# Optimization experiments

Hardware: AMD Instinct MI355X
Metric: run time of the kernel (lower is better)

Reference implementation:

```python
import jax, jax.numpy as jnp
import numpy as np

B, T, D, H = 4, 2048, 1024, 16
HD = D // H  # head dim = 64


def setup_inputs() -> dict:
    key = jax.random.key(0)
    ks = jax.random.split(key, 12)
    s = 1.0 / np.sqrt(D)
    inp = {
        "Q": jax.random.normal(ks[0], (B, T, D), jnp.float32),
        "K": jax.random.normal(ks[1], (B, T, D), jnp.float32),
        "V": jax.random.normal(ks[2], (B, T, D), jnp.float32),
        "mask": jnp.tril(jnp.ones((T, T), jnp.int32))[None, None],  # causal [1,1,T,T]
        "Wq": jax.random.normal(ks[3], (D, D), jnp.float32) * s,
        "bq": jax.random.normal(ks[4], (D,), jnp.float32) * s,
        "Wk": jax.random.normal(ks[5], (D, D), jnp.float32) * s,
        "bk": jax.random.normal(ks[6], (D,), jnp.float32) * s,
        "Wv": jax.random.normal(ks[7], (D, D), jnp.float32) * s,
        "bv": jax.random.normal(ks[8], (D,), jnp.float32) * s,
        "Wo": jax.random.normal(ks[9], (D, D), jnp.float32) * s,
        "bo": jax.random.normal(ks[10], (D,), jnp.float32) * s,
    }
    return inp


def reference(Q, K, V, mask, Wq, bq, Wk, bk, Wv, bv, Wo, bo):
    b, t, d = Q.shape
    # projections (torch Linear: x @ W^T + b)
    q = (Q @ Wq.T + bq).reshape(b, t, H, HD).transpose(0, 2, 1, 3)  # [b,h,t,hd]
    k = (K @ Wk.T + bk).reshape(b, t, H, HD).transpose(0, 2, 1, 3)
    v = (V @ Wv.T + bv).reshape(b, t, H, HD).transpose(0, 2, 1, 3)
    score = jnp.einsum("bhqd,bhkd->bhqk", q, k) / jnp.sqrt(jnp.float32(HD))
    score = jnp.where(mask == 0, jnp.float32(-1e9), score)
    attn = jax.nn.softmax(score, axis=-1)
    out = jnp.einsum("bhqk,bhkd->bhqd", attn, v)
    out = out.transpose(0, 2, 1, 3).reshape(b, t, d)
    return out @ Wo.T + bo
```

## Files before the change

### kernel.cpp

```cpp
#include <hip/hip_runtime.h>
#include <stdint.h>

#define B_SZ  4
#define T_SEQ 2048
#define DIM   1024
#define NH    16
#define HD    64
#define M_TOT (B_SZ * T_SEQ)

typedef unsigned short u16;
typedef unsigned long long u64;
typedef __attribute__((ext_vector_type(8))) __bf16 bf16x8;
typedef __attribute__((ext_vector_type(4))) float  floatx4;
typedef __attribute__((ext_vector_type(16))) float floatx16;

#define SCL_Q (0.125f * 1.44269504089f)

__device__ __forceinline__ u16 f2bf(float f) {
  union { float f; uint32_t u; } v; v.f = f;
  uint32_t r = v.u + 0x7fffu + ((v.u >> 16) & 1u);
  return (u16)(r >> 16);
}

__device__ __forceinline__ void gl_lds16(const void* g, void* l) {
  __builtin_amdgcn_global_load_lds(
      (const __attribute__((address_space(1))) uint32_t*)g,
      (__attribute__((address_space(3))) uint32_t*)l, 16, 0, 0);
}

__global__ __launch_bounds__(256) void cvt_all(
    const float* __restrict__ s0, const float* __restrict__ s1,
    const float* __restrict__ s2, const float* __restrict__ s3,
    const float* __restrict__ s4, const float* __restrict__ s5,
    const float* __restrict__ s6,
    u16* __restrict__ d0, u16* __restrict__ d1, u16* __restrict__ d2,
    u16* __restrict__ d3, u16* __restrict__ d4, u16* __restrict__ d5,
    u16* __restrict__ d6) {
  const float* s; u16* d; int n;
  switch (blockIdx.y) {
    case 0: s = s0; d = d0; n = DIM * DIM; break;
    case 1: s = s1; d = d1; n = DIM * DIM; break;
    case 2: s = s2; d = d2; n = DIM * DIM; break;
    case 3: s = s3; d = d3; n = DIM * DIM; break;
    case 4: s = s4; d = d4; n = M_TOT * DIM; break;
    case 5: s = s5; d = d5; n = M_TOT * DIM; break;
    default: s = s6; d = d6; n = M_TOT * DIM; break;
  }
  int i = (blockIdx.x * 256 + threadIdx.x) * 8;
  if (i >= n) return;
  float4 a = *(const float4*)(s + i);
  float4 b = *(const float4*)(s + i + 4);
  uint4 o;
  o.x = (uint32_t)f2bf(a.x) | ((uint32_t)f2bf(a.y) << 16);
  o.y = (uint32_t)f2bf(a.z) | ((uint32_t)f2bf(a.w) << 16);
  o.z = (uint32_t)f2bf(b.x) | ((uint32_t)f2bf(b.y) << 16);
  o.w = (uint32_t)f2bf(b.z) | ((uint32_t)f2bf(b.w) << 16);
  *(uint4*)(d + i) = o;
}

#define BKG 64
__global__ __launch_bounds__(256) void gemm_qkv(
    const u16* __restrict__ Qb, const u16* __restrict__ Kb,
    const u16* __restrict__ Vb,
    const u16* __restrict__ Wq, const u16* __restrict__ Wk,
    const u16* __restrict__ Wv,
    const float* __restrict__ bq, const float* __restrict__ bk,
    const float* __restrict__ bv,
    u16* __restrict__ qo, u16* __restrict__ ko, u16* __restrict__ vo) {
  const u16* A; const u16* Bw; const float* bias; u16* Co;
  if (blockIdx.z == 0)      { A = Qb; Bw = Wq; bias = bq; Co = qo; }
  else if (blockIdx.z == 1) { A = Kb; Bw = Wk; bias = bk; Co = ko; }
  else                      { A = Vb; Bw = Wv; bias = bv; Co = vo; }

  __shared__ u16 As[128 * 64];
  __shared__ u16 Bs[128 * 64];

  const int tid  = threadIdx.x;
  const int wave = tid >> 6, lane = tid & 63;
  const int quad = lane >> 4, l16 = lane & 15;
  const int wm = wave >> 1, wn = wave & 1;
  const int m0 = blockIdx.x * 128, n0 = blockIdx.y * 128;

  const floatx4 FZ = {0.f, 0.f, 0.f, 0.f};
  floatx4 acc[4][4];
#pragma unroll
  for (int mt = 0; mt < 4; ++mt)
#pragma unroll
    for (int nt = 0; nt < 4; ++nt) acc[mt][nt] = FZ;

  for (int k0 = 0; k0 < DIM; k0 += BKG) {
    __syncthreads();
#pragma unroll
    for (int j = 0; j < 4; ++j) {
      int pc = j * 256 + tid;
      int r = pc >> 3, c = pc & 7;
      int sc = c ^ (r & 7);
      gl_lds16(A  + (size_t)(m0 + r) * DIM + k0 + sc * 8,
               &As[(j * 256 + wave * 64) * 8]);
      gl_lds16(Bw + (size_t)(n0 + r) * DIM + k0 + sc * 8,
               &Bs[(j * 256 + wave * 64) * 8]);
    }
    __syncthreads();

#pragma unroll
    for (int kk = 0; kk < 2; ++kk) {
      bf16x8 af[4], bfr[4];
#pragma unroll
      for (int mt = 0; mt < 4; ++mt) {
        int ra = wm * 64 + mt * 16 + l16;
        af[mt] = *(const bf16x8*)&As[ra * 64 + (((kk * 4 + quad) ^ (ra & 7)) * 8)];
      }
#pragma unroll
      for (int nt = 0; nt < 4; ++nt) {
        int rb = wn * 64 + nt * 16 + l16;
        bfr[nt] = *(const bf16x8*)&Bs[rb * 64 + (((kk * 4 + quad) ^ (rb & 7)) * 8)];
      }
#pragma unroll
      for (int mt = 0; mt < 4; ++mt)
#pragma unroll
        for (int nt = 0; nt < 4; ++nt)
          acc[mt][nt] = __builtin_amdgcn_mfma_f32_16x16x32_bf16(
              af[mt], bfr[nt], acc[mt][nt], 0, 0, 0);
    }
  }

  if (blockIdx.z == 2) {
#pragma unroll
    for (int nt = 0; nt < 4; ++nt) {
      int n = n0 + wn * 64 + nt * 16 + l16;
      float bb = bias[n];
      int h = n >> 6, hd = n & 63;
#pragma unroll
      for (int mt = 0; mt < 4; ++mt) {
        int mbase = m0 + wm * 64 + mt * 16 + quad * 4;
        int b = mbase >> 11, t = mbase & (T_SEQ - 1);
        u64 pk = 0;
#pragma unroll
        for (int r = 0; r < 4; ++r)
          pk |= (u64)f2bf(acc[mt][nt][r] + bb) << (16 * r);
        *(u64*)&Co[((size_t)((b * NH + h) * HD + hd)) * T_SEQ + t] = pk;
      }
    }
  } else {
    const float sc = (blockIdx.z == 0) ? SCL_Q : 1.0f;
#pragma unroll
    for (int nt = 0; nt < 4; ++nt) {
      int n = n0 + wn * 64 + nt * 16 + l16;
      float bb = bias[n];
      int h = n >> 6, hd = n & 63;
#pragma unroll
      for (int mt = 0; mt < 4; ++mt) {
#pragma unroll
        for (int r = 0; r < 4; ++r) {
          int m = m0 + wm * 64 + mt * 16 + quad * 4 + r;
          int b = m >> 11, t = m & (T_SEQ - 1);
          Co[((size_t)(b * NH + h) * T_SEQ + t) * HD + hd] =
              f2bf((acc[mt][nt][r] + bb) * sc);
        }
      }
    }
  }
}

__global__ __launch_bounds__(512, 2) void flash_attn(
    const u16* __restrict__ qp, const u16* __restrict__ kp,
    const u16* __restrict__ vp, u16* __restrict__ ao) {
  const int bh = blockIdx.x;
  const int y = blockIdx.y;
  const int qt = (y < 4) ? (7 - y) : (y - 4);
  const int b = bh >> 4, h = bh & 15;
  const u16* Qg = qp + (size_t)bh * T_SEQ * HD;
  const u16* Kg = kp + (size_t)bh * T_SEQ * HD;
  const u16* Vg = vp + (size_t)bh * HD * T_SEQ;

  __shared__ u16 lds[6][64 * 64];

  const int tid = threadIdx.x, wave = tid >> 6, lane = tid & 63;
  const int hi = lane >> 5, c31 = lane & 31;
  const int lr8 = lane >> 3, lc8 = lane & 7;

  const int qrow = qt * 256 + wave * 32 + c31;

  bf16x8 bq[4];
#pragma unroll
  for (int cth = 0; cth < 4; ++cth)
    bq[cth] = *(const bf16x8*)(Qg + (size_t)qrow * HD + cth * 16 + hi * 8);

  const int nkb = 4 * qt + 4;
  const int srow = wave * 8 + lr8;
  const int ssc = lc8 ^ (srow & 7);

  gl_lds16(Kg + (size_t)srow * HD + ssc * 8, &lds[0][wave * 8 * 64]);
  gl_lds16(Vg + (size_t)srow * T_SEQ + ssc * 8, &lds[1][wave * 8 * 64]);
  gl_lds16(Kg + (size_t)(64 + srow) * HD + ssc * 8, &lds[2][wave * 8 * 64]);
  gl_lds16(Vg + (size_t)srow * T_SEQ + 64 + ssc * 8, &lds[3][wave * 8 * 64]);

  asm volatile("" :: "v"(bq[0]), "v"(bq[1]), "v"(bq[2]), "v"(bq[3]));

  floatx16 o0, o1;
#pragma unroll
  for (int i = 0; i < 16; ++i) { o0[i] = 0.f; o1[i] = 0.f; }
  float l_p = 0.f;

  int koff[4];
#pragma unroll
  for (int x = 0; x < 4; ++x)
    koff[x] = c31 * 64 + (((x * 2 + hi) ^ (c31 & 7)) * 8);

  const int qwmin = qt * 256 + wave * 32;
  const int qwmax = qwmin + 31;
  int pc_ = 0;
  int ps_ = 2;
  for (int kb = 0; kb < nkb; ++kb) {
    if (kb + 1 < nkb) asm volatile("s_waitcnt vmcnt(2)" ::: "memory");
    else              asm volatile("s_waitcnt vmcnt(0)" ::: "memory");
    __builtin_amdgcn_s_barrier();
    __builtin_amdgcn_sched_barrier(0);

    if (kb + 2 < nkb) {
      const u16* Kgk = Kg + (size_t)(kb + 2) * 64 * HD;
      const u16* Vgk = Vg + (size_t)(kb + 2) * 64;
      gl_lds16(Kgk + (size_t)srow * HD + ssc * 8, &lds[ps_ * 2][wave * 8 * 64]);
      gl_lds16(Vgk + (size_t)srow * T_SEQ + ssc * 8,
               &lds[ps_ * 2 + 1][wave * 8 * 64]);
      ps_ = (ps_ == 2) ? 0 : ps_ + 1;
    }

    if (kb * 64 <= qwmax) {
      const u16* Ks = &lds[pc_ * 2][0];
      const u16* Vs = &lds[pc_ * 2 + 1][0];

      floatx16 s0, s1;
#pragma unroll
      for (int i = 0; i < 16; ++i) { s0[i] = 0.f; s1[i] = 0.f; }
#pragma unroll
      for (int cth = 0; cth < 4; ++cth) {
        bf16x8 ka = *(const bf16x8*)&Ks[koff[cth]];
        bf16x8 kb2 = *(const bf16x8*)&Ks[koff[cth] + 32 * 64];
        s0 = __builtin_amdgcn_mfma_f32_32x32x16_bf16(ka, bq[cth], s0, 0, 0, 0);
        s1 = __builtin_amdgcn_mfma_f32_32x32x16_bf16(kb2, bq[cth], s1, 0, 0, 0);
      }

      if (kb * 64 + 63 > qwmin) {
        int kvb = kb * 64 + 4 * hi;
#pragma unroll
        for (int r = 0; r < 16; ++r) {
          int kvr = kvb + (r & 3) + 8 * (r >> 2);
          if (kvr > qrow)      s0[r] = -3e38f;
          if (kvr + 32 > qrow) s1[r] = -3e38f;
        }
      }

      uint32_t pk0[8], pk1[8];
      float rs = 0.f;
#pragma unroll
      for (int rr = 0; rr < 8; ++rr) {
        union { float f; uint32_t u; } x0, x1, y0, y1;
        x0.f = __builtin_amdgcn_exp2f(s0[2 * rr]);
        x1.f = __builtin_amdgcn_exp2f(s0[2 * rr + 1]);
        y0.f = __builtin_amdgcn_exp2f(s1[2 * rr]);
        y1.f = __builtin_amdgcn_exp2f(s1[2 * rr + 1]);
        rs += (x0.f + x1.f) + (y0.f + y1.f);
        pk0[rr] = __builtin_amdgcn_perm(x1.u, x0.u, 0x07060302);
        pk1[rr] = __builtin_amdgcn_perm(y1.u, y0.u, 0x07060302);
      }
      l_p += rs;

#pragma unroll
      for (int cc = 0; cc < 4; ++cc) {
        const uint32_t* pks = (cc & 2) ? pk1 : pk0;
        const int e4 = (cc & 1) * 4;
        auto r0 = __builtin_amdgcn_permlane32_swap(pks[e4 + 0], pks[e4 + 2],
                                                   false, false);
        auto r1 = __builtin_amdgcn_permlane32_swap(pks[e4 + 1], pks[e4 + 3],
                                                   false, false);
        union { uint32_t u[4]; bf16x8 v; } bp;
        bp.u[0] = r0[0]; bp.u[1] = r1[0]; bp.u[2] = r0[1]; bp.u[3] = r1[1];
        bf16x8 va = *(const bf16x8*)&Vs[koff[cc]];
        bf16x8 vb = *(const bf16x8*)&Vs[koff[cc] + 32 * 64];
        o0 = __builtin_amdgcn_mfma_f32_32x32x16_bf16(va, bp.v, o0, 0, 0, 0);
        o1 = __builtin_amdgcn_mfma_f32_32x32x16_bf16(vb, bp.v, o1, 0, 0, 0);
      }
    }
    pc_ = (pc_ == 2) ? 0 : pc_ + 1;
  }

  {
    float l = l_p + __shfl_xor(l_p, 32);
    float inv = 1.0f / l;
    const size_t obase = (size_t)(b * T_SEQ + qrow) * DIM + h * HD;
#pragma unroll
    for (int u4 = 0; u4 < 4; ++u4) {
      u64 w0 = 0, w1 = 0;
#pragma unroll
      for (int r = 0; r < 4; ++r) {
        w0 |= (u64)f2bf(o0[4 * u4 + r] * inv) << (16 * r);
        w1 |= (u64)f2bf(o1[4 * u4 + r] * inv) << (16 * r);
      }
      *(u64*)&ao[obase + 8 * u4 + 4 * hi] = w0;
      *(u64*)&ao[obase + 32 + 8 * u4 + 4 * hi] = w1;
    }
  }
}

__global__ __launch_bounds__(256) void gemm_out(
    const u16* __restrict__ Ain, const u16* __restrict__ Wo,
    const float* __restrict__ bo, float* __restrict__ out) {
  __shared__ u16 As[128 * 64];
  __shared__ u16 Bs[128 * 64];

  const int tid  = threadIdx.x;
  const int wave = tid >> 6, lane = tid & 63;
  const int quad = lane >> 4, l16 = lane & 15;
  const int wm = wave >> 1, wn = wave & 1;
  const int m0 = blockIdx.x * 128, n0 = blockIdx.y * 128;

  const floatx4 FZ = {0.f, 0.f, 0.f, 0.f};
  floatx4 acc[4][4];
#pragma unroll
  for (int mt = 0; mt < 4; ++mt)
#pragma unroll
    for (int nt = 0; nt < 4; ++nt) acc[mt][nt] = FZ;

  for (int k0 = 0; k0 < DIM; k0 += BKG) {
    __syncthreads();
#pragma unroll
    for (int j = 0; j < 4; ++j) {
      int pc = j * 256 + tid;
      int r = pc >> 3, c = pc & 7;
      int sc = c ^ (r & 7);
      gl_lds16(Ain + (size_t)(m0 + r) * DIM + k0 + sc * 8,
               &As[(j * 256 + wave * 64) * 8]);
      gl_lds16(Wo  + (size_t)(n0 + r) * DIM + k0 + sc * 8,
               &Bs[(j * 256 + wave * 64) * 8]);
    }
    __syncthreads();

#pragma unroll
    for (int kk = 0; kk < 2; ++kk) {
      bf16x8 af[4], bfr[4];
#pragma unroll
      for (int mt = 0; mt < 4; ++mt) {
        int ra = wm * 64 + mt * 16 + l16;
        af[mt] = *(const bf16x8*)&As[ra * 64 + (((kk * 4 + quad) ^ (ra & 7)) * 8)];
      }
#pragma unroll
      for (int nt = 0; nt < 4; ++nt) {
        int rb = wn * 64 + nt * 16 + l16;
        bfr[nt] = *(const bf16x8*)&Bs[rb * 64 + (((kk * 4 + quad) ^ (rb & 7)) * 8)];
      }
#pragma unroll
      for (int mt = 0; mt < 4; ++mt)
#pragma unroll
        for (int nt = 0; nt < 4; ++nt)
          acc[mt][nt] = __builtin_amdgcn_mfma_f32_16x16x32_bf16(
              af[mt], bfr[nt], acc[mt][nt], 0, 0, 0);
    }
  }

#pragma unroll
  for (int nt = 0; nt < 4; ++nt) {
    int n = n0 + wn * 64 + nt * 16 + l16;
    float bb = bo[n];
#pragma unroll
    for (int mt = 0; mt < 4; ++mt)
#pragma unroll
      for (int r = 0; r < 4; ++r) {
        int m = m0 + wm * 64 + mt * 16 + quad * 4 + r;
        out[(size_t)m * DIM + n] = acc[mt][nt][r] + bb;
      }
  }
}

extern "C" void kernel_launch(void* const* d_in, const int* in_sizes, int n_in,
                              void* d_out, int out_size, void* d_ws,
                              size_t ws_size, hipStream_t stream) {
  const float* Q  = (const float*)d_in[0];
  const float* K  = (const float*)d_in[1];
  const float* V  = (const float*)d_in[2];
  const float* Wq = (const float*)d_in[4];
  const float* bq = (const float*)d_in[5];
  const float* Wk = (const float*)d_in[6];
  const float* bk = (const float*)d_in[7];
  const float* Wv = (const float*)d_in[8];
  const float* bv = (const float*)d_in[9];
  const float* Wo = (const float*)d_in[10];
  const float* bo = (const float*)d_in[11];
  float* out = (float*)d_out;

  u16* wqb = (u16*)d_ws;
  u16* wkb = wqb + 1048576;
  u16* wvb = wkb + 1048576;
  u16* wob = wvb + 1048576;
  u16* Qb  = wob + 1048576;
  u16* Kb  = Qb + (size_t)M_TOT * DIM;
  u16* Vb  = Kb + (size_t)M_TOT * DIM;
  u16* qp  = Vb + (size_t)M_TOT * DIM;
  u16* kp  = qp + (size_t)M_TOT * DIM;
  u16* vp  = kp + (size_t)M_TOT * DIM;
  u16* aop = vp + (size_t)M_TOT * DIM;

  cvt_all<<<dim3(M_TOT * DIM / 2048, 7), 256, 0, stream>>>(
      Wq, Wk, Wv, Wo, Q, K, V, wqb, wkb, wvb, wob, Qb, Kb, Vb);

  gemm_qkv<<<dim3(M_TOT / 128, DIM / 128, 3), 256, 0, stream>>>(
      Qb, Kb, Vb, wqb, wkb, wvb, bq, bk, bv, qp, kp, vp);

  flash_attn<<<dim3(B_SZ * NH, T_SEQ / 256), 512, 0, stream>>>(qp, kp, vp, aop);

  gemm_out<<<dim3(M_TOT / 128, DIM / 128), 256, 0, stream>>>(aop, wob, bo, out);
}
```

Measured before the change: 309.2 us.

## Rewrite QKV projection GEMM with 256x256 tiles and double-buffered async prefetch

The QKV projection GEMM moves from 128x128 tiles with 256 threads and a load-sync-compute loop to 256x256 tiles with 512 threads. It now double-buffers LDS for A and B and issues global-to-LDS loads for the next K-steps while the current step's MFMAs run. Each K-step is split into four phases with explicit barriers, waitcnts and setprio, meant to hide memory latency and raise operand reuse per loaded byte. In exchange it uses 128KB of LDS per block and launches only 384 blocks, which risks poor CU fill and a partial last wave.

Measured after the change: 324.3 us. 4.9% more time.

```diff
diff --git a/kernel.cpp b/kernel.cpp
--- a/kernel.cpp
+++ b/kernel.cpp
@@ -58,8 +58,22 @@
   *(uint4*)(d + i) = o;
 }
 
-#define BKG 64
-__global__ __launch_bounds__(256) void gemm_qkv(
+#define BKG  64
+#define NT_K (DIM / BKG)
+
+__device__ __forceinline__ void stage_half(
+    const u16* __restrict__ src, int grow0, int k0, u16* ldsbase,
+    int wave, int lr8, int lc8) {
+#pragma unroll
+  for (int j = 0; j < 2; ++j) {
+    int rb = j * 64 + wave * 8;
+    int R  = grow0 + rb + lr8;
+    gl_lds16(src + (size_t)R * DIM + k0 + ((lc8 ^ lr8) * 8),
+             ldsbase + (size_t)rb * 64);
+  }
+}
+
+__global__ __launch_bounds__(512, 2) void gemm_qkv(
     const u16* __restrict__ Qb, const u16* __restrict__ Kb,
     const u16* __restrict__ Vb,
     const u16* __restrict__ Wq, const u16* __restrict__ Wk,
@@ -72,55 +86,97 @@
   else if (blockIdx.z == 1) { A = Kb; Bw = Wk; bias = bk; Co = ko; }
   else                      { A = Vb; Bw = Wv; bias = bv; Co = vo; }
 
-  __shared__ u16 As[128 * 64];
-  __shared__ u16 Bs[128 * 64];
+  __shared__ u16 sh[4 * 256 * 64];
+  u16* const Ab0 = sh;
+  u16* const Ab1 = sh + 256 * 64;
+  u16* const Bb0 = sh + 2 * 256 * 64;
+  u16* const Bb1 = sh + 3 * 256 * 64;
 
   const int tid  = threadIdx.x;
   const int wave = tid >> 6, lane = tid & 63;
   const int quad = lane >> 4, l16 = lane & 15;
-  const int wm = wave >> 1, wn = wave & 1;
-  const int m0 = blockIdx.x * 128, n0 = blockIdx.y * 128;
+  const int lr8 = lane >> 3, lc8 = lane & 7;
+  const int wm = wave >> 2, wn = wave & 3;
+  const int m0 = blockIdx.x * 256, n0 = blockIdx.y * 256;
 
   const floatx4 FZ = {0.f, 0.f, 0.f, 0.f};
-  floatx4 acc[4][4];
-#pragma unroll
-  for (int mt = 0; mt < 4; ++mt)
+  floatx4 acc[8][4];
+#pragma unroll
+  for (int mt = 0; mt < 8; ++mt)
 #pragma unroll
     for (int nt = 0; nt < 4; ++nt) acc[mt][nt] = FZ;
 
-  for (int k0 = 0; k0 < DIM; k0 += BKG) {
-    __syncthreads();
-#pragma unroll
-    for (int j = 0; j < 4; ++j) {
-      int pc = j * 256 + tid;
-      int r = pc >> 3, c = pc & 7;
-      int sc = c ^ (r & 7);
-      gl_lds16(A  + (size_t)(m0 + r) * DIM + k0 + sc * 8,
-               &As[(j * 256 + wave * 64) * 8]);
-      gl_lds16(Bw + (size_t)(n0 + r) * DIM + k0 + sc * 8,
-               &Bs[(j * 256 + wave * 64) * 8]);
-    }
-    __syncthreads();
-
-#pragma unroll
-    for (int kk = 0; kk < 2; ++kk) {
-      bf16x8 af[4], bfr[4];
-#pragma unroll
-      for (int mt = 0; mt < 4; ++mt) {
-        int ra = wm * 64 + mt * 16 + l16;
-        af[mt] = *(const bf16x8*)&As[ra * 64 + (((kk * 4 + quad) ^ (ra & 7)) * 8)];
-      }
-#pragma unroll
-      for (int nt = 0; nt < 4; ++nt) {
-        int rb = wn * 64 + nt * 16 + l16;
-        bfr[nt] = *(const bf16x8*)&Bs[rb * 64 + (((kk * 4 + quad) ^ (rb & 7)) * 8)];
-      }
+  stage_half(A,  m0,       0,   Ab0,            wave, lr8, lc8);
+  stage_half(A,  m0 + 128, 0,   Ab0 + 128 * 64, wave, lr8, lc8);
+  stage_half(Bw, n0,       0,   Bb0,            wave, lr8, lc8);
+  stage_half(Bw, n0 + 128, 0,   Bb0 + 128 * 64, wave, lr8, lc8);
+  stage_half(A,  m0,       BKG, Ab1,            wave, lr8, lc8);
+  stage_half(A,  m0 + 128, BKG, Ab1 + 128 * 64, wave, lr8, lc8);
+  asm volatile("s_waitcnt vmcnt(4)" ::: "memory");
+  __builtin_amdgcn_s_barrier();
+  __builtin_amdgcn_sched_barrier(0);
+
+  bf16x8 afr[4][2];
+  bf16x8 bfr[2][2];
+
+  for (int t = 0; t < NT_K; ++t) {
+    u16* const Ac = (t & 1) ? Ab1 : Ab0;
+    u16* const Bc = (t & 1) ? Bb1 : Bb0;
+    u16* const An = (t & 1) ? Ab1 : Ab0;
+    u16* const Bn = (t & 1) ? Bb0 : Bb1;
+
+#pragma unroll
+    for (int ph = 0; ph < 4; ++ph) {
+      const int mq = ph >> 1, nq = ph & 1;
+      if (nq == 0) {
+#pragma unroll
+        for (int mt = 0; mt < 4; ++mt) {
+          int ra = wm * 128 + mq * 64 + mt * 16 + l16;
+#pragma unroll
+          for (int kk = 0; kk < 2; ++kk)
+            afr[mt][kk] = *(const bf16x8*)
+                &Ac[ra * 64 + (((kk * 4 + quad) ^ (ra & 7)) * 8)];
+        }
+      }
+#pragma unroll
+      for (int nt = 0; nt < 2; ++nt) {
+        int rb = wn * 64 + nq * 32 + nt * 16 + l16;
+#pragma unroll
+        for (int kk = 0; kk < 2; ++kk)
+          bfr[nt][kk] = *(const bf16x8*)
+              &Bc[rb * 64 + (((kk * 4 + quad) ^ (rb & 7)) * 8)];
+      }
+      if (ph == 0 && t + 1 < NT_K)
+        stage_half(Bw, n0,       (t + 1) * BKG, Bn,            wave, lr8, lc8);
+      if (ph == 1 && t + 1 < NT_K)
+        stage_half(Bw, n0 + 128, (t + 1) * BKG, Bn + 128 * 64, wave, lr8, lc8);
+      if (ph == 3 && t + 2 < NT_K) {
+        stage_half(A, m0,       (t + 2) * BKG, An,            wave, lr8, lc8);
+        stage_half(A, m0 + 128, (t + 2) * BKG, An + 128 * 64, wave, lr8, lc8);
+      }
+      __builtin_amdgcn_s_barrier();
+      __builtin_amdgcn_sched_barrier(0);
+      asm volatile("s_waitcnt lgkmcnt(0)" ::: "memory");
+      __builtin_amdgcn_sched_barrier(0);
+      __builtin_amdgcn_s_setprio(1);
 #pragma unroll
       for (int mt = 0; mt < 4; ++mt)
 #pragma unroll
-        for (int nt = 0; nt < 4; ++nt)
-          acc[mt][nt] = __builtin_amdgcn_mfma_f32_16x16x32_bf16(
-              af[mt], bfr[nt], acc[mt][nt], 0, 0, 0);
+        for (int nt = 0; nt < 2; ++nt)
+#pragma unroll
+          for (int kk = 0; kk < 2; ++kk)
+            acc[mq * 4 + mt][nq * 2 + nt] =
+                __builtin_amdgcn_mfma_f32_16x16x32_bf16(
+                    afr[mt][kk], bfr[nt][kk], acc[mq * 4 + mt][nq * 2 + nt],
+                    0, 0, 0);
+      __builtin_amdgcn_s_setprio(0);
+      if (ph == 3) {
+        if (t + 1 >= NT_K) break;
+        if (t + 2 < NT_K) asm volatile("s_waitcnt vmcnt(4)" ::: "memory");
+        else              asm volatile("s_waitcnt vmcnt(0)" ::: "memory");
+      }
+      __builtin_amdgcn_s_barrier();
+      __builtin_amdgcn_sched_barrier(0);
     }
   }
 
@@ -129,16 +185,16 @@
     for (int nt = 0; nt < 4; ++nt) {
       int n = n0 + wn * 64 + nt * 16 + l16;
       float bb = bias[n];
-      int h = n >> 6, hd = n & 63;
-#pragma unroll
-      for (int mt = 0; mt < 4; ++mt) {
-        int mbase = m0 + wm * 64 + mt * 16 + quad * 4;
-        int b = mbase >> 11, t = mbase & (T_SEQ - 1);
+      int hh = n >> 6, hd = n & 63;
+#pragma unroll
+      for (int mt = 0; mt < 8; ++mt) {
+        int mbase = m0 + wm * 128 + mt * 16 + quad * 4;
+        int b = mbase >> 11, tq = mbase & (T_SEQ - 1);
         u64 pk = 0;
 #pragma unroll
         for (int r = 0; r < 4; ++r)
           pk |= (u64)f2bf(acc[mt][nt][r] + bb) << (16 * r);
-        *(u64*)&Co[((size_t)((b * NH + h) * HD + hd)) * T_SEQ + t] = pk;
+        *(u64*)&Co[((size_t)((b * NH + hh) * HD + hd)) * T_SEQ + tq] = pk;
       }
     }
   } else {
@@ -147,14 +203,14 @@
     for (int nt = 0; nt < 4; ++nt) {
       int n = n0 + wn * 64 + nt * 16 + l16;
       float bb = bias[n];
-      int h = n >> 6, hd = n & 63;
-#pragma unroll
-      for (int mt = 0; mt < 4; ++mt) {
+      int hh = n >> 6, hd = n & 63;
+#pragma unroll
+      for (int mt = 0; mt < 8; ++mt) {
 #pragma unroll
         for (int r = 0; r < 4; ++r) {
-          int m = m0 + wm * 64 + mt * 16 + quad * 4 + r;
-          int b = m >> 11, t = m & (T_SEQ - 1);
-          Co[((size_t)(b * NH + h) * T_SEQ + t) * HD + hd] =
+          int m = m0 + wm * 128 + mt * 16 + quad * 4 + r;
+          int b = m >> 11, tq = m & (T_SEQ - 1);
+          Co[((size_t)(b * NH + hh) * T_SEQ + tq) * HD + hd] =
               f2bf((acc[mt][nt][r] + bb) * sc);
         }
       }
@@ -403,7 +459,7 @@
   cvt_all<<<dim3(M_TOT * DIM / 2048, 7), 256, 0, stream>>>(
       Wq, Wk, Wv, Wo, Q, K, V, wqb, wkb, wvb, wob, Qb, Kb, Vb);
 
-  gemm_qkv<<<dim3(M_TOT / 128, DIM / 128, 3), 256, 0, stream>>>(
+  gemm_qkv<<<dim3(M_TOT / 256, DIM / 256, 3), 512, 0, stream>>>(
       Qb, Kb, Vb, wqb, wkb, wvb, bq, bk, bv, qp, kp, vp);
 
   flash_attn<<<dim3(B_SZ * NH, T_SEQ / 256), 512, 0, stream>>>(qp, kp, vp, aop);
```

## Process two 32-row query tiles per wave in flash attention, halving waves

Applied to the files above, without the earlier changes.

Each wave of the flash attention kernel now handles 64 query rows (two 32-row MFMA tiles) instead of 32, and the block shrinks from 512 to 256 threads. Every K and V fragment read from LDS then feeds four MFMAs instead of two, which halves LDS read traffic per unit of compute and halves barrier participants. Each thread now issues two K/V staging loads per buffer. The cost is roughly double the accumulator and score registers per wave, which may cut occupancy or cause spills, and fewer waves per block to hide latency.

After: 308.2 us (median of 3 runs). About the same (-0.3%).

```diff
diff --git a/kernel.cpp b/kernel.cpp
--- a/kernel.cpp
+++ b/kernel.cpp
@@ -162,7 +162,7 @@
   }
 }
 
-__global__ __launch_bounds__(512, 2) void flash_attn(
+__global__ __launch_bounds__(256, 2) void flash_attn(
     const u16* __restrict__ qp, const u16* __restrict__ kp,
     const u16* __restrict__ vp, u16* __restrict__ ao) {
   const int bh = blockIdx.x;
@@ -179,126 +179,164 @@
   const int hi = lane >> 5, c31 = lane & 31;
   const int lr8 = lane >> 3, lc8 = lane & 7;
 
-  const int qrow = qt * 256 + wave * 32 + c31;
-
-  bf16x8 bq[4];
-#pragma unroll
-  for (int cth = 0; cth < 4; ++cth)
-    bq[cth] = *(const bf16x8*)(Qg + (size_t)qrow * HD + cth * 16 + hi * 8);
+  const int wbase = qt * 256 + wave * 64;
+  const int qrowA = wbase + c31;
+  const int qrowB = qrowA + 32;
+
+  bf16x8 bqA[4], bqB[4];
+#pragma unroll
+  for (int cth = 0; cth < 4; ++cth) {
+    bqA[cth] = *(const bf16x8*)(Qg + (size_t)qrowA * HD + cth * 16 + hi * 8);
+    bqB[cth] = *(const bf16x8*)(Qg + (size_t)qrowB * HD + cth * 16 + hi * 8);
+  }
 
   const int nkb = 4 * qt + 4;
-  const int srow = wave * 8 + lr8;
-  const int ssc = lc8 ^ (srow & 7);
-
-  gl_lds16(Kg + (size_t)srow * HD + ssc * 8, &lds[0][wave * 8 * 64]);
-  gl_lds16(Vg + (size_t)srow * T_SEQ + ssc * 8, &lds[1][wave * 8 * 64]);
-  gl_lds16(Kg + (size_t)(64 + srow) * HD + ssc * 8, &lds[2][wave * 8 * 64]);
-  gl_lds16(Vg + (size_t)srow * T_SEQ + 64 + ssc * 8, &lds[3][wave * 8 * 64]);
-
-  asm volatile("" :: "v"(bq[0]), "v"(bq[1]), "v"(bq[2]), "v"(bq[3]));
-
-  floatx16 o0, o1;
-#pragma unroll
-  for (int i = 0; i < 16; ++i) { o0[i] = 0.f; o1[i] = 0.f; }
-  float l_p = 0.f;
+
+#define STAGE_KV(kbidx, bufpair)                                              \
+  {                                                                           \
+    const u16* Kgk = Kg + (size_t)(kbidx) * 64 * HD;                          \
+    const u16* Vgk = Vg + (size_t)(kbidx) * 64;                               \
+    _Pragma("unroll") for (int i_ = 0; i_ < 2; ++i_) {                        \
+      int r_ = i_ * 32 + wave * 8 + lr8;                                      \
+      int sc_ = lc8 ^ (r_ & 7);                                               \
+      gl_lds16(Kgk + (size_t)r_ * HD + sc_ * 8,                               \
+               &lds[(bufpair) * 2][(i_ * 32 + wave * 8) * 64]);               \
+      gl_lds16(Vgk + (size_t)r_ * T_SEQ + sc_ * 8,                            \
+               &lds[(bufpair) * 2 + 1][(i_ * 32 + wave * 8) * 64]);           \
+    }                                                                         \
+  }
+
+  STAGE_KV(0, 0);
+  STAGE_KV(1, 1);
+
+  asm volatile("" :: "v"(bqA[0]), "v"(bqA[1]), "v"(bqA[2]), "v"(bqA[3]),
+                     "v"(bqB[0]), "v"(bqB[1]), "v"(bqB[2]), "v"(bqB[3]));
+
+  floatx16 oA0, oA1, oB0, oB1;
+#pragma unroll
+  for (int i = 0; i < 16; ++i) { oA0[i] = 0.f; oA1[i] = 0.f;
+                                 oB0[i] = 0.f; oB1[i] = 0.f; }
+  float l_pA = 0.f, l_pB = 0.f;
 
   int koff[4];
 #pragma unroll
   for (int x = 0; x < 4; ++x)
     koff[x] = c31 * 64 + (((x * 2 + hi) ^ (c31 & 7)) * 8);
 
-  const int qwmin = qt * 256 + wave * 32;
-  const int qwmax = qwmin + 31;
-  int pc_ = 0;
-  int ps_ = 2;
+  int pcb = 0;
+  int psb = 2;
   for (int kb = 0; kb < nkb; ++kb) {
-    if (kb + 1 < nkb) asm volatile("s_waitcnt vmcnt(2)" ::: "memory");
+    if (kb + 1 < nkb) asm volatile("s_waitcnt vmcnt(4)" ::: "memory");
     else              asm volatile("s_waitcnt vmcnt(0)" ::: "memory");
     __builtin_amdgcn_s_barrier();
     __builtin_amdgcn_sched_barrier(0);
 
     if (kb + 2 < nkb) {
-      const u16* Kgk = Kg + (size_t)(kb + 2) * 64 * HD;
-      const u16* Vgk = Vg + (size_t)(kb + 2) * 64;
-      gl_lds16(Kgk + (size_t)srow * HD + ssc * 8, &lds[ps_ * 2][wave * 8 * 64]);
-      gl_lds16(Vgk + (size_t)srow * T_SEQ + ssc * 8,
-               &lds[ps_ * 2 + 1][wave * 8 * 64]);
-      ps_ = (ps_ == 2) ? 0 : ps_ + 1;
-    }
-
-    if (kb * 64 <= qwmax) {
-      const u16* Ks = &lds[pc_ * 2][0];
-      const u16* Vs = &lds[pc_ * 2 + 1][0];
-
-      floatx16 s0, s1;
-#pragma unroll
-      for (int i = 0; i < 16; ++i) { s0[i] = 0.f; s1[i] = 0.f; }
+      STAGE_KV(kb + 2, psb);
+      psb = (psb == 2) ? 0 : psb + 1;
+    }
+
+    if (kb * 64 <= wbase + 63) {
+      const u16* Ks = &lds[pcb * 2][0];
+      const u16* Vs = &lds[pcb * 2 + 1][0];
+
+      floatx16 sA0, sA1, sB0, sB1;
+#pragma unroll
+      for (int i = 0; i < 16; ++i) { sA0[i] = 0.f; sA1[i] = 0.f;
+                                     sB0[i] = 0.f; sB1[i] = 0.f; }
 #pragma unroll
       for (int cth = 0; cth < 4; ++cth) {
         bf16x8 ka = *(const bf16x8*)&Ks[koff[cth]];
-        bf16x8 kb2 = *(const bf16x8*)&Ks[koff[cth] + 32 * 64];
-        s0 = __builtin_amdgcn_mfma_f32_32x32x16_bf16(ka, bq[cth], s0, 0, 0, 0);
-        s1 = __builtin_amdgcn_mfma_f32_32x32x16_bf16(kb2, bq[cth], s1, 0, 0, 0);
-      }
-
-      if (kb * 64 + 63 > qwmin) {
+        bf16x8 kh = *(const bf16x8*)&Ks[koff[cth] + 32 * 64];
+        sA0 = __builtin_amdgcn_mfma_f32_32x32x16_bf16(ka, bqA[cth], sA0, 0, 0, 0);
+        sA1 = __builtin_amdgcn_mfma_f32_32x32x16_bf16(kh, bqA[cth], sA1, 0, 0, 0);
+        sB0 = __builtin_amdgcn_mfma_f32_32x32x16_bf16(ka, bqB[cth], sB0, 0, 0, 0);
+        sB1 = __builtin_amdgcn_mfma_f32_32x32x16_bf16(kh, bqB[cth], sB1, 0, 0, 0);
+      }
+
+      if (kb * 64 + 63 > wbase) {
         int kvb = kb * 64 + 4 * hi;
 #pragma unroll
         for (int r = 0; r < 16; ++r) {
           int kvr = kvb + (r & 3) + 8 * (r >> 2);
-          if (kvr > qrow)      s0[r] = -3e38f;
-          if (kvr + 32 > qrow) s1[r] = -3e38f;
+          if (kvr > qrowA)      sA0[r] = -3e38f;
+          if (kvr + 32 > qrowA) sA1[r] = -3e38f;
+          if (kvr > qrowB)      sB0[r] = -3e38f;
+          if (kvr + 32 > qrowB) sB1[r] = -3e38f;
         }
       }
 
-      uint32_t pk0[8], pk1[8];
-      float rs = 0.f;
+      uint32_t pkA0[8], pkA1[8], pkB0[8], pkB1[8];
+      float rsA = 0.f, rsB = 0.f;
 #pragma unroll
       for (int rr = 0; rr < 8; ++rr) {
         union { float f; uint32_t u; } x0, x1, y0, y1;
-        x0.f = __builtin_amdgcn_exp2f(s0[2 * rr]);
-        x1.f = __builtin_amdgcn_exp2f(s0[2 * rr + 1]);
-        y0.f = __builtin_amdgcn_exp2f(s1[2 * rr]);
-        y1.f = __builtin_amdgcn_exp2f(s1[2 * rr + 1]);
-        rs += (x0.f + x1.f) + (y0.f + y1.f);
-        pk0[rr] = __builtin_amdgcn_perm(x1.u, x0.u, 0x07060302);
-        pk1[rr] = __builtin_amdgcn_perm(y1.u, y0.u, 0x07060302);
-      }
-      l_p += rs;
+        x0.f = __builtin_amdgcn_exp2f(sA0[2 * rr]);
+        x1.f = __builtin_amdgcn_exp2f(sA0[2 * rr + 1]);
+        y0.f = __builtin_amdgcn_exp2f(sA1[2 * rr]);
+        y1.f = __builtin_amdgcn_exp2f(sA1[2 * rr + 1]);
+        rsA += (x0.f + x1.f) + (y0.f + y1.f);
+        pkA0[rr] = __builtin_amdgcn_perm(x1.u, x0.u, 0x07060302);
+        pkA1[rr] = __builtin_amdgcn_perm(y1.u, y0.u, 0x07060302);
+        x0.f = __builtin_amdgcn_exp2f(sB0[2 * rr]);
+        x1.f = __builtin_amdgcn_exp2f(sB0[2 * rr + 1]);
+        y0.f = __builtin_amdgcn_exp2f(sB1[2 * rr]);
+        y1.f = __builtin_amdgcn_exp2f(sB1[2 * rr + 1]);
+        rsB += (x0.f + x1.f) + (y0.f + y1.f);
+        pkB0[rr] = __builtin_amdgcn_perm(x1.u, x0.u, 0x07060302);
+        pkB1[rr] = __builtin_amdgcn_perm(y1.u, y0.u, 0x07060302);
+      }
+      l_pA += rsA;
+      l_pB += rsB;
 
 #pragma unroll
       for (int cc = 0; cc < 4; ++cc) {
-        const uint32_t* pks = (cc & 2) ? pk1 : pk0;
+        const uint32_t* pA = (cc & 2) ? pkA1 : pkA0;
+        const uint32_t* pB = (cc & 2) ? pkB1 : pkB0;
         const int e4 = (cc & 1) * 4;
-        auto r0 = __builtin_amdgcn_permlane32_swap(pks[e4 + 0], pks[e4 + 2],
+        auto a0 = __builtin_amdgcn_permlane32_swap(pA[e4 + 0], pA[e4 + 2],
                                                    false, false);
-        auto r1 = __builtin_amdgcn_permlane32_swap(pks[e4 + 1], pks[e4 + 3],
+        auto a1 = __builtin_amdgcn_permlane32_swap(pA[e4 + 1], pA[e4 + 3],
                                                    false, false);
-        union { uint32_t u[4]; bf16x8 v; } bp;
-        bp.u[0] = r0[0]; bp.u[1] = r1[0]; bp.u[2] = r0[1]; bp.u[3] = r1[1];
+        auto b0 = __builtin_amdgcn_permlane32_swap(pB[e4 + 0], pB[e4 + 2],
+                                                   false, false);
+        auto b1 = __builtin_amdgcn_permlane32_swap(pB[e4 + 1], pB[e4 + 3],
+                                                   false, false);
+        union { uint32_t u[4]; bf16x8 v; } bpA, bpB;
+        bpA.u[0] = a0[0]; bpA.u[1] = a1[0]; bpA.u[2] = a0[1]; bpA.u[3] = a1[1];
+        bpB.u[0] = b0[0]; bpB.u[1] = b1[0]; bpB.u[2] = b0[1]; bpB.u[3] = b1[1];
         bf16x8 va = *(const bf16x8*)&Vs[koff[cc]];
         bf16x8 vb = *(const bf16x8*)&Vs[koff[cc] + 32 * 64];
-        o0 = __builtin_amdgcn_mfma_f32_32x32x16_bf16(va, bp.v, o0, 0, 0, 0);
-        o1 = __builtin_amdgcn_mfma_f32_32x32x16_bf16(vb, bp.v, o1, 0, 0, 0);
-      }
-    }
-    pc_ = (pc_ == 2) ? 0 : pc_ + 1;
-  }
+        oA0 = __builtin_amdgcn_mfma_f32_32x32x16_bf16(va, bpA.v, oA0, 0, 0, 0);
+        oA1 = __builtin_amdgcn_mfma_f32_32x32x16_bf16(vb, bpA.v, oA1, 0, 0, 0);
+        oB0 = __builtin_amdgcn_mfma_f32_32x32x16_bf16(va, bpB.v, oB0, 0, 0, 0);
+        oB1 = __builtin_amdgcn_mfma_f32_32x32x16_bf16(vb, bpB.v, oB1, 0, 0, 0);
+      }
+    }
+    pcb = (pcb == 2) ? 0 : pcb + 1;
+  }
+#undef STAGE_KV
 
   {
-    float l = l_p + __shfl_xor(l_p, 32);
-    float inv = 1.0f / l;
-    const size_t obase = (size_t)(b * T_SEQ + qrow) * DIM + h * HD;
+    float lA = l_pA + __shfl_xor(l_pA, 32);
+    float lB = l_pB + __shfl_xor(l_pB, 32);
+    float invA = 1.0f / lA, invB = 1.0f / lB;
+    const size_t obaseA = (size_t)(b * T_SEQ + qrowA) * DIM + h * HD;
+    const size_t obaseB = obaseA + (size_t)32 * DIM;
 #pragma unroll
     for (int u4 = 0; u4 < 4; ++u4) {
-      u64 w0 = 0, w1 = 0;
+      u64 wA0 = 0, wA1 = 0, wB0 = 0, wB1 = 0;
 #pragma unroll
       for (int r = 0; r < 4; ++r) {
-        w0 |= (u64)f2bf(o0[4 * u4 + r] * inv) << (16 * r);
-        w1 |= (u64)f2bf(o1[4 * u4 + r] * inv) << (16 * r);
-      }
-      *(u64*)&ao[obase + 8 * u4 + 4 * hi] = w0;
-      *(u64*)&ao[obase + 32 + 8 * u4 + 4 * hi] = w1;
+        wA0 |= (u64)f2bf(oA0[4 * u4 + r] * invA) << (16 * r);
+        wA1 |= (u64)f2bf(oA1[4 * u4 + r] * invA) << (16 * r);
+        wB0 |= (u64)f2bf(oB0[4 * u4 + r] * invB) << (16 * r);
+        wB1 |= (u64)f2bf(oB1[4 * u4 + r] * invB) << (16 * r);
+      }
+      *(u64*)&ao[obaseA + 8 * u4 + 4 * hi] = wA0;
+      *(u64*)&ao[obaseA + 32 + 8 * u4 + 4 * hi] = wA1;
+      *(u64*)&ao[obaseB + 8 * u4 + 4 * hi] = wB0;
+      *(u64*)&ao[obaseB + 32 + 8 * u4 + 4 * hi] = wB1;
     }
   }
 }
@@ -406,7 +444,7 @@
   gemm_qkv<<<dim3(M_TOT / 128, DIM / 128, 3), 256, 0, stream>>>(
       Qb, Kb, Vb, wqb, wkb, wvb, bq, bk, bv, qp, kp, vp);
 
-  flash_attn<<<dim3(B_SZ * NH, T_SEQ / 256), 512, 0, stream>>>(qp, kp, vp, aop);
+  flash_attn<<<dim3(B_SZ * NH, T_SEQ / 256), 256, 0, stream>>>(qp, kp, vp, aop);
 
   gemm_out<<<dim3(M_TOT / 128, DIM / 128), 256, 0, stream>>>(aop, wob, bo, out);
 }
```
